# Performance work log

Hardware: AMD Instinct MI355X
Metric: run time of the kernel (lower is better)

Reference implementation:

```python
import jax, jax.numpy as jnp
import numpy as np
import math

D_MODEL = 1024
N_DEVICES = 64
HIDDEN = 128
N_HEADS = 8
B, S = 16, 1024
W_SCALE = 0.02

def setup_inputs() -> dict:
    key = jax.random.key(0)
    ks = jax.random.split(key, 24)
    f = jax.random.normal
    inp = {
        'x': f(ks[0], (B, S, D_MODEL), jnp.float32),
        # attention pooling (n_heads=8, non-causal, self-attention) weights, stored [in,out]
        'wq': f(ks[1], (D_MODEL, D_MODEL), jnp.float32) * W_SCALE,
        'bq': jnp.zeros((D_MODEL,), jnp.float32),
        'wk': f(ks[2], (D_MODEL, D_MODEL), jnp.float32) * W_SCALE,
        'bk': jnp.zeros((D_MODEL,), jnp.float32),
        'wv': f(ks[3], (D_MODEL, D_MODEL), jnp.float32) * W_SCALE,
        'bv': jnp.zeros((D_MODEL,), jnp.float32),
        'wo': f(ks[4], (D_MODEL, D_MODEL), jnp.float32) * W_SCALE,
        'bo': jnp.zeros((D_MODEL,), jnp.float32),
        # device embedding table
        'emb': f(ks[5], (N_DEVICES, D_MODEL), jnp.float32),
        # routing gate: Linear(2d,d) -> Tanh -> Linear(d,N) -> Softmax
        'rg_w1': f(ks[6], (2 * D_MODEL, D_MODEL), jnp.float32) * W_SCALE,
        'rg_b1': jnp.zeros((D_MODEL,), jnp.float32),
        'rg_w2': f(ks[7], (D_MODEL, N_DEVICES), jnp.float32) * W_SCALE,
        'rg_b2': jnp.zeros((N_DEVICES,), jnp.float32),
        'reg_w1': f(ks[8], (N_DEVICES, D_MODEL, HIDDEN), jnp.float32) * W_SCALE,
        'reg_b1': jnp.zeros((N_DEVICES, HIDDEN), jnp.float32),
        'reg_w2': f(ks[9], (N_DEVICES, HIDDEN), jnp.float32) * W_SCALE,
        'reg_b2': jnp.zeros((N_DEVICES,), jnp.float32),
        # stacked per-device classification heads: Linear(d,h)->ReLU->Linear(h,1)->Sigmoid
        'cls_w1': f(ks[10], (N_DEVICES, D_MODEL, HIDDEN), jnp.float32) * W_SCALE,
        'cls_b1': jnp.zeros((N_DEVICES, HIDDEN), jnp.float32),
        'cls_w2': f(ks[11], (N_DEVICES, HIDDEN), jnp.float32) * W_SCALE,
        'cls_b2': jnp.zeros((N_DEVICES,), jnp.float32),
    }
    return inp


def _forward(x, wq, bq, wk, bk, wv, bv, wo, bo, emb,
             rg_w1, rg_b1, rg_w2, rg_b2,
             reg_w1, reg_b1, reg_w2, reg_b2,
             cls_w1, cls_b1, cls_w2, cls_b2):
    b, s, d = x.shape
    dk = d // N_HEADS
    scale = 1.0 / math.sqrt(dk)

    def split_heads(t):  # [b,s,d] -> [b,h,s,dk]
        return t.reshape(b, s, N_HEADS, dk).transpose(0, 2, 1, 3)

    Q = split_heads(x @ wq + bq)
    K = split_heads(x @ wk + bk)
    V = split_heads(x @ wv + bv)
    scores = jnp.einsum('bhqd,bhkd->bhqk', Q, K) * scale
    attn = jax.nn.softmax(scores, axis=-1)  # non-causal, no mask, eval (no dropout)
    ctx = jnp.einsum('bhqk,bhkd->bhqd', attn, V)
    ctx = ctx.transpose(0, 2, 1, 3).reshape(b, s, d)
    pooled = ctx @ wo + bo                       # [b,s,d]
    g = pooled.mean(axis=1)                      # [b,d] global_repr

    g_exp = jnp.broadcast_to(g[:, None, :], (b, N_DEVICES, d))
    de_exp = jnp.broadcast_to(emb[None, :, :], (b, N_DEVICES, d))

    # routing gate
    ri = jnp.concatenate([g_exp, de_exp], axis=-1)        # [b,N,2d]
    h = jnp.tanh(ri @ rg_w1 + rg_b1)                      # [b,N,d]
    rw = jax.nn.softmax(h @ rg_w2 + rg_b2, axis=-1)       # [b,N,N]
    device_repr = jnp.einsum('bnm,md->bnd', rw, emb)      # bmm with expanded embeds
    combined = g_exp + device_repr                        # [b,N,d]

    hr = jax.nn.relu(jnp.einsum('bnd,ndh->bnh', combined, reg_w1) + reg_b1)
    reg = jax.nn.softplus(jnp.einsum('bnh,nh->bn', hr, reg_w2) + reg_b2)

    # per-device classification heads (stacked)
    hc = jax.nn.relu(jnp.einsum('bnd,ndh->bnh', combined, cls_w1) + cls_b1)
    cls = jax.nn.sigmoid(jnp.einsum('bnh,nh->bn', hc, cls_w2) + cls_b2)
    return reg, cls


def reference(x, wq, bq, wk, bk, wv, bv, wo, bo, emb,
              rg_w1, rg_b1, rg_w2, rg_b2,
              reg_w1, reg_b1, reg_w2, reg_b2,
              cls_w1, cls_b1, cls_w2, cls_b2):
    return _forward(x, wq, bq, wk, bk, wv, bv, wo, bo, emb,
                    rg_w1, rg_b1, rg_w2, rg_b2,
                    reg_w1, reg_b1, reg_w2, reg_b2,
                    cls_w1, cls_b1, cls_w2, cls_b2)
```

## Files before the change

### kernel.cpp

```cpp
#include <hip/hip_runtime.h>

typedef unsigned short ushort_t;
typedef __attribute__((ext_vector_type(8))) short short8;
typedef __attribute__((ext_vector_type(4))) float floatx4;

__device__ __forceinline__ ushort_t f2bf(float f) {
    unsigned u = __float_as_uint(f);
    return (ushort_t)((u + 0x7fffu + ((u >> 16) & 1u)) >> 16);
}
__device__ __forceinline__ void gll16(const void* g, void* l) {
    __builtin_amdgcn_global_load_lds(
        (const __attribute__((address_space(1))) unsigned int*)g,
        (__attribute__((address_space(3))) unsigned int*)l, 16, 0, 0);
}
#if __has_builtin(__builtin_amdgcn_exp2f)
#define EXP2f(x) __builtin_amdgcn_exp2f(x)
#else
#define EXP2f(x) exp2f(x)
#endif

__global__ void prep_kernel(const float* __restrict__ x, ushort_t* __restrict__ xb) {
    size_t i = ((size_t)blockIdx.x * 256 + threadIdx.x) * 8;
    float4 v0 = *(const float4*)(x + i);
    float4 v1 = *(const float4*)(x + i + 4);
    uint4 o;
    o.x = (unsigned)f2bf(v0.x) | ((unsigned)f2bf(v0.y) << 16);
    o.y = (unsigned)f2bf(v0.z) | ((unsigned)f2bf(v0.w) << 16);
    o.z = (unsigned)f2bf(v1.x) | ((unsigned)f2bf(v1.y) << 16);
    o.w = (unsigned)f2bf(v1.z) | ((unsigned)f2bf(v1.w) << 16);
    *(uint4*)(xb + i) = o;
}

__global__ __launch_bounds__(256) void transpose_kernel(
    const float* __restrict__ wq, const float* __restrict__ wk,
    ushort_t* __restrict__ wqT, ushort_t* __restrict__ wkT)
{
    const float* src = blockIdx.z ? wk : wq;
    ushort_t* dst = blockIdx.z ? wkT : wqT;
    const int k0 = blockIdx.x * 64, n0 = blockIdx.y * 64;
    __shared__ float t[64][65];
    const int tid = threadIdx.x;
    const int rr = tid >> 4, cc = (tid & 15) * 4;
#pragma unroll
    for (int p = 0; p < 4; ++p) {
        float4 v = *(const float4*)(src + (size_t)(k0 + p * 16 + rr) * 1024 + n0 + cc);
        t[p * 16 + rr][cc + 0] = v.x;
        t[p * 16 + rr][cc + 1] = v.y;
        t[p * 16 + rr][cc + 2] = v.z;
        t[p * 16 + rr][cc + 3] = v.w;
    }
    __syncthreads();
#pragma unroll
    for (int p = 0; p < 4; ++p) {
        int nl = p * 16 + rr;
        uint2 o;
        o.x = (unsigned)f2bf(t[cc + 0][nl]) | ((unsigned)f2bf(t[cc + 1][nl]) << 16);
        o.y = (unsigned)f2bf(t[cc + 2][nl]) | ((unsigned)f2bf(t[cc + 3][nl]) << 16);
        *(uint2*)(dst + (size_t)(n0 + nl) * 1024 + k0 + cc) = o;
    }
}

__global__ __launch_bounds__(256) void gemm_qk_kernel(
    const ushort_t* __restrict__ xb, const ushort_t* __restrict__ wqT, const ushort_t* __restrict__ wkT,
    const float* __restrict__ bq, const float* __restrict__ bk,
    ushort_t* __restrict__ Qb, ushort_t* __restrict__ Kb)
{
    const int bm = blockIdx.x;
    const int bn = blockIdx.y;
    const int mat = blockIdx.z;
    const ushort_t* W = mat ? wkT : wqT;
    const float* bias = mat ? bk : bq;
    ushort_t* Out = mat ? Kb : Qb;
    const float postscale = mat ? 1.0f : 0.12751744900508692f;

    __shared__ ushort_t a_lds[2][128 * 32];
    __shared__ ushort_t b_lds[2][128 * 32];

    const int tid = threadIdx.x;
    const int lane = tid & 63;
    const int wave = tid >> 6;
    const int wr = wave >> 1, wc = wave & 1;
    const int l16 = lane & 15, quad = lane >> 4;
    const int qs = quad ^ ((l16 >> 1) & 3);

    floatx4 acc[4][4];
    const floatx4 zero4 = {0.f, 0.f, 0.f, 0.f};
#pragma unroll
    for (int i = 0; i < 4; ++i)
#pragma unroll
        for (int j = 0; j < 4; ++j) acc[i][j] = zero4;

    const int srow = wave * 32 + (lane >> 2);
    const int skof = ((lane & 3) ^ ((lane >> 3) & 3)) * 8;
    const ushort_t* gA = xb + (size_t)(bm * 128 + srow) * 1024 + skof;
    const ushort_t* gB = W + (size_t)(bn * 128 + srow) * 1024 + skof;

    auto issue = [&](int buf, int k0) {
        ushort_t* lA = &a_lds[buf][wave * 1024];
        ushort_t* lB = &b_lds[buf][wave * 1024];
        gll16(gA + k0, lA);
        gll16(gA + k0 + 16 * 1024, lA + 512);
        gll16(gB + k0, lB);
        gll16(gB + k0 + 16 * 1024, lB + 512);
    };

    auto compute = [&](int buf) {
        const ushort_t* la = a_lds[buf];
        const ushort_t* lb = b_lds[buf];
        short8 afr[4], bfr[4];
#pragma unroll
        for (int mi = 0; mi < 4; ++mi)
            afr[mi] = *(const short8*)&la[(wr * 64 + mi * 16 + l16) * 32 + qs * 8];
#pragma unroll
        for (int ni = 0; ni < 4; ++ni)
            bfr[ni] = *(const short8*)&lb[(wc * 64 + ni * 16 + l16) * 32 + qs * 8];
#pragma unroll
        for (int mi = 0; mi < 4; ++mi)
#pragma unroll
            for (int ni = 0; ni < 4; ++ni)
                acc[mi][ni] = __builtin_amdgcn_mfma_f32_16x16x32_bf16(afr[mi], bfr[ni], acc[mi][ni], 0, 0, 0);
    };

    issue(0, 0);
#pragma unroll 4
    for (int kt = 0; kt < 31; ++kt) {
        __syncthreads();
        issue((kt + 1) & 1, (kt + 1) * 32);
        compute(kt & 1);
    }
    __syncthreads();
    compute(1);

    const int bq_ = bm >> 3;
    const int sb = (bm & 7) * 128 + wr * 64 + quad * 4;
    const int dc = wc * 64 + l16;
    float bp[4];
#pragma unroll
    for (int ni = 0; ni < 4; ++ni) bp[ni] = bias[bn * 128 + dc + ni * 16] * postscale;
    ushort_t* ob = Out + ((size_t)(bq_ * 8 + bn) * 1024 + sb) * 128 + dc;
#pragma unroll
    for (int mi = 0; mi < 4; ++mi)
#pragma unroll
        for (int ni = 0; ni < 4; ++ni) {
            ushort_t* p = ob + mi * 2048 + ni * 16;
#pragma unroll
            for (int r = 0; r < 4; ++r)
                p[r * 128] = f2bf(fmaf(acc[mi][ni][r], postscale, bp[ni]));
        }
}

__global__ __launch_bounds__(256, 4) void attn_mfma_kernel(
    const ushort_t* __restrict__ Qb,
    const ushort_t* __restrict__ Kb,
    float* __restrict__ wout)
{
    const int bh = blockIdx.x;
    const int qt = blockIdx.y;
    __shared__ ushort_t ks[2][64 * 128];

    const int tid = threadIdx.x;
    const int wave = tid >> 6, lane = tid & 63;
    const int l16 = lane & 15, quad = lane >> 4;

    const ushort_t* Ksrc = Kb + (size_t)bh * 1024 * 128;

    int srcoff[4];
#pragma unroll
    for (int c = 0; c < 4; ++c) {
        int r = wave * 16 + c * 4 + (lane >> 4);
        int g = (lane & 15) ^ (r & 15);
        srcoff[c] = r * 128 + g * 8;
    }

    auto issue = [&](int buf, int kt) {
        const ushort_t* src = Ksrc + (size_t)kt * 8192;
#pragma unroll
        for (int c = 0; c < 4; ++c)
            gll16(src + srcoff[c], &ks[buf][(wave * 4 + c) * 512]);
    };

    short8 aq[2][4];
    {
        const ushort_t* qsrc = Qb + ((size_t)bh * 1024 + qt * 128 + wave * 32) * 128;
#pragma unroll
        for (int mi = 0; mi < 2; ++mi)
#pragma unroll
            for (int ksp = 0; ksp < 4; ++ksp)
                aq[mi][ksp] = *(const short8*)(qsrc + (size_t)(mi * 16 + l16) * 128 + ksp * 32 + quad * 8);
    }

    const floatx4 zero4 = {0.f, 0.f, 0.f, 0.f};
    float lsum[2][4];
#pragma unroll
    for (int mi = 0; mi < 2; ++mi)
#pragma unroll
        for (int r = 0; r < 4; ++r) lsum[mi][r] = 0.f;

    issue(0, 0);

    for (int kt = 0; kt < 16; ++kt) {
        __syncthreads();
        if (kt < 15) issue((kt + 1) & 1, kt + 1);
        const ushort_t* kbuf = ks[kt & 1];
        floatx4 acc[2][4];
#pragma unroll
        for (int mi = 0; mi < 2; ++mi)
#pragma unroll
            for (int ni = 0; ni < 4; ++ni) acc[mi][ni] = zero4;
#pragma unroll
        for (int ksp = 0; ksp < 4; ++ksp) {
            short8 bk[4];
#pragma unroll
            for (int ni = 0; ni < 4; ++ni) {
                int n = ni * 16 + l16;
                int gs = (ksp * 4 + quad) ^ (n & 15);
                bk[ni] = *(const short8*)&kbuf[n * 128 + gs * 8];
            }
#pragma unroll
            for (int mi = 0; mi < 2; ++mi)
#pragma unroll
                for (int ni = 0; ni < 4; ++ni)
                    acc[mi][ni] = __builtin_amdgcn_mfma_f32_16x16x32_bf16(aq[mi][ksp], bk[ni], acc[mi][ni], 0, 0, 0);
        }
#pragma unroll
        for (int mi = 0; mi < 2; ++mi)
#pragma unroll
            for (int r = 0; r < 4; ++r) {
                float s = 0.f;
#pragma unroll
                for (int ni = 0; ni < 4; ++ni) s += EXP2f(acc[mi][ni][r]);
                lsum[mi][r] += s;
            }
    }

    issue(0, 0);

    float invl[2][4];
#pragma unroll
    for (int mi = 0; mi < 2; ++mi)
#pragma unroll
        for (int r = 0; r < 4; ++r) {
            float s = lsum[mi][r];
#pragma unroll
            for (int off = 1; off < 16; off <<= 1) s += __shfl_xor(s, off, 16);
            invl[mi][r] = 1.f / s;
        }

    for (int kt = 0; kt < 16; ++kt) {
        __syncthreads();
        if (kt < 15) issue((kt + 1) & 1, kt + 1);
        const ushort_t* kbuf = ks[kt & 1];
        floatx4 acc[2][4];
#pragma unroll
        for (int mi = 0; mi < 2; ++mi)
#pragma unroll
            for (int ni = 0; ni < 4; ++ni) acc[mi][ni] = zero4;
#pragma unroll
        for (int ksp = 0; ksp < 4; ++ksp) {
            short8 bk[4];
#pragma unroll
            for (int ni = 0; ni < 4; ++ni) {
                int n = ni * 16 + l16;
                int gs = (ksp * 4 + quad) ^ (n & 15);
                bk[ni] = *(const short8*)&kbuf[n * 128 + gs * 8];
            }
#pragma unroll
            for (int mi = 0; mi < 2; ++mi)
#pragma unroll
                for (int ni = 0; ni < 4; ++ni)
                    acc[mi][ni] = __builtin_amdgcn_mfma_f32_16x16x32_bf16(aq[mi][ksp], bk[ni], acc[mi][ni], 0, 0, 0);
        }
#pragma unroll
        for (int ni = 0; ni < 4; ++ni) {
            float s = 0.f;
#pragma unroll
            for (int mi = 0; mi < 2; ++mi)
#pragma unroll
                for (int r = 0; r < 4; ++r)
                    s += EXP2f(acc[mi][ni][r]) * invl[mi][r];
            s += __shfl_xor(s, 16, 64);
            s += __shfl_xor(s, 32, 64);
            if (quad == 0) atomicAdd(&wout[bh * 1024 + kt * 64 + ni * 16 + l16], s);
        }
    }
}

__global__ __launch_bounds__(256) void u_kernel(const ushort_t* __restrict__ xb,
                                                const float* __restrict__ w,
                                                float* __restrict__ u)
{
    const int b = blockIdx.x, kc = blockIdx.y;
    const int c4 = threadIdx.x;
    const ushort_t* Xp = xb + ((size_t)(b * 1024 + kc * 64)) * 1024 + c4 * 4;
    float4 acc[8];
#pragma unroll
    for (int h = 0; h < 8; ++h) acc[h] = make_float4(0.f, 0.f, 0.f, 0.f);
    const float* wb = w + b * 8 * 1024 + kc * 64;
    for (int k = 0; k < 64; ++k) {
        uint2 uv = *(const uint2*)(Xp + (size_t)k * 1024);
        float x0 = __uint_as_float(uv.x << 16);
        float x1 = __uint_as_float(uv.x & 0xffff0000u);
        float x2 = __uint_as_float(uv.y << 16);
        float x3 = __uint_as_float(uv.y & 0xffff0000u);
#pragma unroll
        for (int h = 0; h < 8; ++h) {
            float ww = wb[h * 1024 + k];
            acc[h].x = fmaf(ww, x0, acc[h].x);
            acc[h].y = fmaf(ww, x1, acc[h].y);
            acc[h].z = fmaf(ww, x2, acc[h].z);
            acc[h].w = fmaf(ww, x3, acc[h].w);
        }
    }
#pragma unroll
    for (int h = 0; h < 8; ++h) {
        float* dst = u + ((size_t)(b * 8 + h)) * 1024 + c4 * 4;
        atomicAdd(dst + 0, acc[h].x);
        atomicAdd(dst + 1, acc[h].y);
        atomicAdd(dst + 2, acc[h].z);
        atomicAdd(dst + 3, acc[h].w);
    }
}

__global__ __launch_bounds__(256) void sgemm_kernel(
    const float* __restrict__ A, int lda, long sAz,
    const float* __restrict__ Bm, int ldb, long sBz,
    const float* __restrict__ bias, long sBiasz,
    float* __restrict__ C, int ldc, long sCz,
    int M, int N, int K, float alpha, int nks)
{
    const int z = blockIdx.z;
    const int ks = blockIdx.x % nks;
    const int mt = blockIdx.x / nks;
    const int Kc = K / nks;
    A += (size_t)z * sAz;
    Bm += (size_t)z * sBz;
    C += (size_t)z * sCz;
    const float* bptr = bias ? bias + (size_t)z * sBiasz : nullptr;
    __shared__ float As[64 * 36];
    __shared__ float Bs[32 * 68];
    const int tid = threadIdx.x;
    const int row0 = mt * 64, col0 = blockIdx.y * 64;
    const int ty = tid >> 4, tx = tid & 15;
    float acc[4][4] = {};
    const int aflat = tid * 8;
    const int ar = aflat >> 5, ac = aflat & 31;
    const int br = aflat >> 6, bc = aflat & 63;
    for (int k0 = ks * Kc; k0 < (ks + 1) * Kc; k0 += 32) {
        __syncthreads();
        float4 va0 = make_float4(0.f, 0.f, 0.f, 0.f), va1 = va0;
        if (row0 + ar < M) {
            const float* src = A + (size_t)(row0 + ar) * lda + k0 + ac;
            va0 = *(const float4*)src;
            va1 = *(const float4*)(src + 4);
        }
        *(float4*)&As[ar * 36 + ac] = va0;
        *(float4*)&As[ar * 36 + ac + 4] = va1;
        {
            const float* srcb = Bm + (size_t)(k0 + br) * ldb + col0 + bc;
            *(float4*)&Bs[br * 68 + bc] = *(const float4*)srcb;
            *(float4*)&Bs[br * 68 + bc + 4] = *(const float4*)(srcb + 4);
        }
        __syncthreads();
#pragma unroll
        for (int kk = 0; kk < 32; ++kk) {
            float a0 = As[(ty * 4 + 0) * 36 + kk];
            float a1 = As[(ty * 4 + 1) * 36 + kk];
            float a2 = As[(ty * 4 + 2) * 36 + kk];
            float a3 = As[(ty * 4 + 3) * 36 + kk];
            float b0 = Bs[kk * 68 + tx * 4 + 0];
            float b1 = Bs[kk * 68 + tx * 4 + 1];
            float b2 = Bs[kk * 68 + tx * 4 + 2];
            float b3 = Bs[kk * 68 + tx * 4 + 3];
            acc[0][0] = fmaf(a0, b0, acc[0][0]); acc[0][1] = fmaf(a0, b1, acc[0][1]);
            acc[0][2] = fmaf(a0, b2, acc[0][2]); acc[0][3] = fmaf(a0, b3, acc[0][3]);
            acc[1][0] = fmaf(a1, b0, acc[1][0]); acc[1][1] = fmaf(a1, b1, acc[1][1]);
            acc[1][2] = fmaf(a1, b2, acc[1][2]); acc[1][3] = fmaf(a1, b3, acc[1][3]);
            acc[2][0] = fmaf(a2, b0, acc[2][0]); acc[2][1] = fmaf(a2, b1, acc[2][1]);
            acc[2][2] = fmaf(a2, b2, acc[2][2]); acc[2][3] = fmaf(a2, b3, acc[2][3]);
            acc[3][0] = fmaf(a3, b0, acc[3][0]); acc[3][1] = fmaf(a3, b1, acc[3][1]);
            acc[3][2] = fmaf(a3, b2, acc[3][2]); acc[3][3] = fmaf(a3, b3, acc[3][3]);
        }
    }
#pragma unroll
    for (int i = 0; i < 4; ++i) {
        int r = row0 + ty * 4 + i;
        if (r >= M) continue;
#pragma unroll
        for (int j = 0; j < 4; ++j) {
            int c = col0 + tx * 4 + j;
            float v = alpha * acc[i][j] + ((bptr && ks == 0) ? bptr[c] : 0.f);
            if (nks > 1) atomicAdd(&C[(size_t)r * ldc + c], v);
            else C[(size_t)r * ldc + c] = v;
        }
    }
}

__global__ __launch_bounds__(256) void gate_kernel(
    const float* __restrict__ Ge, const float* __restrict__ Ee, const float* __restrict__ rg_b1,
    const float* __restrict__ rg_w2, const float* __restrict__ rg_b2,
    const float* __restrict__ emb, float* __restrict__ DR)
{
    const int row = blockIdx.x;
    const int b = row >> 6, n = row & 63;
    __shared__ float h[1024];
    __shared__ float red[256];
    __shared__ float rw[64];
    const int tid = threadIdx.x;
    for (int c = tid; c < 1024; c += 256)
        h[c] = tanhf(Ge[b * 1024 + c] + Ee[n * 1024 + c] + rg_b1[c]);
    __syncthreads();
    const int j = tid & 63, ch = tid >> 6;
    float part = 0.f;
    const float* w2p = rg_w2 + (size_t)(ch * 256) * 64 + j;
    for (int c = 0; c < 256; ++c)
        part = fmaf(h[ch * 256 + c], w2p[c * 64], part);
    red[tid] = part;
    __syncthreads();
    if (tid < 64) {
        float lg = red[tid] + red[tid + 64] + red[tid + 128] + red[tid + 192] + rg_b2[j];
        float m = lg;
#pragma unroll
        for (int off = 1; off < 64; off <<= 1) m = fmaxf(m, __shfl_xor(m, off, 64));
        float e = __expf(lg - m);
        float s = e;
#pragma unroll
        for (int off = 1; off < 64; off <<= 1) s += __shfl_xor(s, off, 64);
        rw[tid] = e / s;
    }
    __syncthreads();
    float4 acc = make_float4(0.f, 0.f, 0.f, 0.f);
    const float4* E4 = (const float4*)emb;
    for (int nn = 0; nn < 64; ++nn) {
        float wv = rw[nn];
        float4 ev = E4[nn * 256 + tid];
        acc.x = fmaf(wv, ev.x, acc.x);
        acc.y = fmaf(wv, ev.y, acc.y);
        acc.z = fmaf(wv, ev.z, acc.z);
        acc.w = fmaf(wv, ev.w, acc.w);
    }
    *(float4*)&DR[(size_t)row * 1024 + tid * 4] = acc;
}

__global__ __launch_bounds__(256) void heads_p1_kernel(
    const float* __restrict__ g, const float* __restrict__ DR,
    const float* __restrict__ rw1, const float* __restrict__ cw1,
    float* __restrict__ hpart)
{
    const int n = blockIdx.x, task = blockIdx.y, ksl = blockIdx.z;
    __shared__ float combs[16 * 128];
    const int tid = threadIdx.x;
    for (int i = tid; i < 2048; i += 256) {
        int b = i >> 7, c = i & 127;
        int gc = ksl * 128 + c;
        combs[i] = g[b * 1024 + gc] + DR[((size_t)(b * 64 + n)) * 1024 + gc];
    }
    __syncthreads();
    const int j = tid & 127, sub = tid >> 7;
    const float* W1 = (task ? cw1 : rw1) + (size_t)n * 131072 + (size_t)ksl * 128 * 128;
    float a[8] = {};
    for (int c4 = 0; c4 < 32; ++c4) {
        const float w0 = W1[(c4 * 4 + 0) * 128 + j];
        const float w1 = W1[(c4 * 4 + 1) * 128 + j];
        const float w2 = W1[(c4 * 4 + 2) * 128 + j];
        const float w3 = W1[(c4 * 4 + 3) * 128 + j];
#pragma unroll
        for (int bb = 0; bb < 8; ++bb) {
            float4 cv = *(const float4*)&combs[(sub * 8 + bb) * 128 + c4 * 4];
            a[bb] = fmaf(cv.x, w0, a[bb]);
            a[bb] = fmaf(cv.y, w1, a[bb]);
            a[bb] = fmaf(cv.z, w2, a[bb]);
            a[bb] = fmaf(cv.w, w3, a[bb]);
        }
    }
    float* dst = hpart + (((size_t)(ksl * 2 + task) * 64 + n) * 16 + sub * 8) * 128 + j;
#pragma unroll
    for (int bb = 0; bb < 8; ++bb) dst[bb * 128] = a[bb];
}

__global__ __launch_bounds__(256) void heads_p2_kernel(
    const float* __restrict__ hpart,
    const float* __restrict__ rb1, const float* __restrict__ rw2, const float* __restrict__ rb2,
    const float* __restrict__ cb1, const float* __restrict__ cw2, const float* __restrict__ cb2,
    float* __restrict__ out)
{
    const int n = blockIdx.x, task = blockIdx.y;
    const int tid = threadIdx.x;
    const int b = tid >> 4, jg = tid & 15;
    const float* b1 = (task ? cb1 : rb1) + n * 128 + jg * 8;
    const float* W2 = (task ? cw2 : rw2) + n * 128 + jg * 8;
    float s = 0.f;
#pragma unroll
    for (int k = 0; k < 8; ++k) {
        float h = b1[k];
#pragma unroll
        for (int ksl = 0; ksl < 8; ++ksl)
            h += hpart[(((size_t)(ksl * 2 + task) * 64 + n) * 16 + b) * 128 + jg * 8 + k];
        s = fmaf(fmaxf(h, 0.f), W2[k], s);
    }
#pragma unroll
    for (int off = 1; off < 16; off <<= 1) s += __shfl_xor(s, off, 16);
    if (jg == 0) {
        s += (task ? cb2 : rb2)[n];
        float r = task ? (1.f / (1.f + __expf(-s)))
                       : (fmaxf(s, 0.f) + log1pf(__expf(-fabsf(s))));
        out[task * 1024 + b * 64 + n] = r;
    }
}

extern "C" void kernel_launch(void* const* d_in, const int* in_sizes, int n_in,
                              void* d_out, int out_size, void* d_ws, size_t ws_size,
                              hipStream_t stream)
{
    const float* x      = (const float*)d_in[0];
    const float* wq     = (const float*)d_in[1];
    const float* bq     = (const float*)d_in[2];
    const float* wk     = (const float*)d_in[3];
    const float* bk     = (const float*)d_in[4];
    const float* wv     = (const float*)d_in[5];
    const float* bv     = (const float*)d_in[6];
    const float* wo     = (const float*)d_in[7];
    const float* bo     = (const float*)d_in[8];
    const float* emb    = (const float*)d_in[9];
    const float* rg_w1  = (const float*)d_in[10];
    const float* rg_b1  = (const float*)d_in[11];
    const float* rg_w2  = (const float*)d_in[12];
    const float* rg_b2  = (const float*)d_in[13];
    const float* reg_w1 = (const float*)d_in[14];
    const float* reg_b1 = (const float*)d_in[15];
    const float* reg_w2 = (const float*)d_in[16];
    const float* reg_b2 = (const float*)d_in[17];
    const float* cls_w1 = (const float*)d_in[18];
    const float* cls_b1 = (const float*)d_in[19];
    const float* cls_w2 = (const float*)d_in[20];
    const float* cls_b2 = (const float*)d_in[21];

    char* ws = (char*)d_ws;
    size_t off = 0;
    auto alloc = [&](size_t bytes) { size_t cur = off; off += (bytes + 255) & ~(size_t)255; return cur; };

    ushort_t* xb  = (ushort_t*)(ws + alloc((size_t)16777216 * 2));
    ushort_t* wqT = (ushort_t*)(ws + alloc((size_t)1048576 * 2));
    ushort_t* wkT = (ushort_t*)(ws + alloc((size_t)1048576 * 2));
    ushort_t* Qb  = (ushort_t*)(ws + alloc((size_t)16777216 * 2));
    ushort_t* Kb  = (ushort_t*)(ws + alloc((size_t)16777216 * 2));
    size_t zero_beg = off;
    float* wcol = (float*)(ws + alloc((size_t)131072 * 4));
    float* u    = (float*)(ws + alloc((size_t)131072 * 4));
    float* cm   = (float*)(ws + alloc((size_t)16384 * 4));
    float* gbuf = (float*)(ws + alloc((size_t)16384 * 4));
    float* Ge   = (float*)(ws + alloc((size_t)16384 * 4));
    float* Ee   = (float*)(ws + alloc((size_t)65536 * 4));
    size_t zero_end = off;
    float* DR    = (float*)(ws + alloc((size_t)1048576 * 4));
    float* hpart = (float*)(ws + alloc((size_t)2097152 * 4));

    hipMemsetAsync(ws + zero_beg, 0, zero_end - zero_beg, stream);

    prep_kernel<<<8192, 256, 0, stream>>>(x, xb);
    transpose_kernel<<<dim3(16, 16, 2), 256, 0, stream>>>(wq, wk, wqT, wkT);
    gemm_qk_kernel<<<dim3(128, 8, 2), 256, 0, stream>>>(xb, wqT, wkT, bq, bk, Qb, Kb);
    attn_mfma_kernel<<<dim3(128, 8), 256, 0, stream>>>(Qb, Kb, wcol);
    u_kernel<<<dim3(16, 16), 256, 0, stream>>>(xb, wcol, u);
    sgemm_kernel<<<dim3(4, 2, 8), 256, 0, stream>>>(u, 8192, 1024, wv, 1024, 128, bv, 128,
                                                    cm, 1024, 128, 16, 128, 1024, 1.f / 1024.f, 4);
    sgemm_kernel<<<dim3(8, 16, 1), 256, 0, stream>>>(cm, 1024, 0, wo, 1024, 0, bo, 0,
                                                     gbuf, 1024, 0, 16, 1024, 1024, 1.f, 8);
    sgemm_kernel<<<dim3(8, 16, 1), 256, 0, stream>>>(gbuf, 1024, 0, rg_w1, 1024, 0, nullptr, 0,
                                                     Ge, 1024, 0, 16, 1024, 1024, 1.f, 8);
    sgemm_kernel<<<dim3(8, 16, 1), 256, 0, stream>>>(emb, 1024, 0, rg_w1 + (size_t)1048576, 1024, 0, nullptr, 0,
                                                     Ee, 1024, 0, 64, 1024, 1024, 1.f, 8);
    gate_kernel<<<1024, 256, 0, stream>>>(Ge, Ee, rg_b1, rg_w2, rg_b2, emb, DR);
    heads_p1_kernel<<<dim3(64, 2, 8), 256, 0, stream>>>(gbuf, DR, reg_w1, cls_w1, hpart);
    heads_p2_kernel<<<dim3(64, 2), 256, 0, stream>>>(hpart, reg_b1, reg_w2, reg_b2,
                                                     cls_b1, cls_w2, cls_b2, (float*)d_out);
    (void)in_sizes; (void)n_in; (void)out_size; (void)ws_size;
}
```

Baseline: 524.9 us.

## Fuse prep/transpose launches, share X tile across Q/K GEMM, widen attention blocks

Merges the x bf16 conversion and the weight transposes into one launch. Rewrites the Q/K projection GEMM as 512-thread blocks that load the x tile once and compute both Q and K, which halves A-tile traffic. Doubles the attention block size to 8 waves covering 256 query rows, so each staged K tile is shared by more queries. Also merges the two routing-gate sgemm launches into one kernel. The cost is higher LDS and register pressure per block and fewer, larger blocks. The attention kernel body beyond the load indexing is not visible, so its consistency with the new 256-row tile cannot be fully checked.

```diff
diff --git a/kernel.cpp b/kernel.cpp
--- a/kernel.cpp
+++ b/kernel.cpp
@@ -19,27 +19,31 @@
 #define EXP2f(x) exp2f(x)
 #endif
 
-__global__ void prep_kernel(const float* __restrict__ x, ushort_t* __restrict__ xb) {
-    size_t i = ((size_t)blockIdx.x * 256 + threadIdx.x) * 8;
-    float4 v0 = *(const float4*)(x + i);
-    float4 v1 = *(const float4*)(x + i + 4);
-    uint4 o;
-    o.x = (unsigned)f2bf(v0.x) | ((unsigned)f2bf(v0.y) << 16);
-    o.y = (unsigned)f2bf(v0.z) | ((unsigned)f2bf(v0.w) << 16);
-    o.z = (unsigned)f2bf(v1.x) | ((unsigned)f2bf(v1.y) << 16);
-    o.w = (unsigned)f2bf(v1.z) | ((unsigned)f2bf(v1.w) << 16);
-    *(uint4*)(xb + i) = o;
-}
-
-__global__ __launch_bounds__(256) void transpose_kernel(
+__global__ __launch_bounds__(256) void prep_tr_kernel(
+    const float* __restrict__ x, ushort_t* __restrict__ xb,
     const float* __restrict__ wq, const float* __restrict__ wk,
     ushort_t* __restrict__ wqT, ushort_t* __restrict__ wkT)
 {
-    const float* src = blockIdx.z ? wk : wq;
-    ushort_t* dst = blockIdx.z ? wkT : wqT;
-    const int k0 = blockIdx.x * 64, n0 = blockIdx.y * 64;
     __shared__ float t[64][65];
-    const int tid = threadIdx.x;
+    const int bid = blockIdx.x;
+    const int tid = threadIdx.x;
+    if (bid < 8192) {
+        size_t i = ((size_t)bid * 256 + tid) * 8;
+        float4 v0 = *(const float4*)(x + i);
+        float4 v1 = *(const float4*)(x + i + 4);
+        uint4 o;
+        o.x = (unsigned)f2bf(v0.x) | ((unsigned)f2bf(v0.y) << 16);
+        o.y = (unsigned)f2bf(v0.z) | ((unsigned)f2bf(v0.w) << 16);
+        o.z = (unsigned)f2bf(v1.x) | ((unsigned)f2bf(v1.y) << 16);
+        o.w = (unsigned)f2bf(v1.z) | ((unsigned)f2bf(v1.w) << 16);
+        *(uint4*)(xb + i) = o;
+        return;
+    }
+    const int b2 = bid - 8192;
+    const int bx = b2 & 15, by = (b2 >> 4) & 15, bz = b2 >> 8;
+    const float* src = bz ? wk : wq;
+    ushort_t* dst = bz ? wkT : wqT;
+    const int k0 = bx * 64, n0 = by * 64;
     const int rr = tid >> 4, cc = (tid & 15) * 4;
 #pragma unroll
     for (int p = 0; p < 4; ++p) {
@@ -60,26 +64,23 @@
     }
 }
 
-__global__ __launch_bounds__(256) void gemm_qk_kernel(
+__global__ __launch_bounds__(512, 4) void gemm_qk_kernel(
     const ushort_t* __restrict__ xb, const ushort_t* __restrict__ wqT, const ushort_t* __restrict__ wkT,
     const float* __restrict__ bq, const float* __restrict__ bk,
     ushort_t* __restrict__ Qb, ushort_t* __restrict__ Kb)
 {
     const int bm = blockIdx.x;
     const int bn = blockIdx.y;
-    const int mat = blockIdx.z;
-    const ushort_t* W = mat ? wkT : wqT;
-    const float* bias = mat ? bk : bq;
-    ushort_t* Out = mat ? Kb : Qb;
-    const float postscale = mat ? 1.0f : 0.12751744900508692f;
 
     __shared__ ushort_t a_lds[2][128 * 32];
-    __shared__ ushort_t b_lds[2][128 * 32];
+    __shared__ ushort_t q_lds[2][128 * 32];
+    __shared__ ushort_t k_lds[2][128 * 32];
 
     const int tid = threadIdx.x;
     const int lane = tid & 63;
     const int wave = tid >> 6;
-    const int wr = wave >> 1, wc = wave & 1;
+    const int wmat = wave >> 2;
+    const int wr = (wave >> 1) & 1, wc = wave & 1;
     const int l16 = lane & 15, quad = lane >> 4;
     const int qs = quad ^ ((l16 >> 1) & 3);
 
@@ -90,23 +91,24 @@
 #pragma unroll
         for (int j = 0; j < 4; ++j) acc[i][j] = zero4;
 
-    const int srow = wave * 32 + (lane >> 2);
-    const int skof = ((lane & 3) ^ ((lane >> 3) & 3)) * 8;
+    const int srow = tid >> 2;
+    const int skof = ((tid & 3) ^ ((tid >> 3) & 3)) * 8;
     const ushort_t* gA = xb + (size_t)(bm * 128 + srow) * 1024 + skof;
-    const ushort_t* gB = W + (size_t)(bn * 128 + srow) * 1024 + skof;
+    const ushort_t* gQ = wqT + (size_t)(bn * 128 + srow) * 1024 + skof;
+    const ushort_t* gK = wkT + (size_t)(bn * 128 + srow) * 1024 + skof;
 
     auto issue = [&](int buf, int k0) {
-        ushort_t* lA = &a_lds[buf][wave * 1024];
-        ushort_t* lB = &b_lds[buf][wave * 1024];
-        gll16(gA + k0, lA);
-        gll16(gA + k0 + 16 * 1024, lA + 512);
-        gll16(gB + k0, lB);
-        gll16(gB + k0 + 16 * 1024, lB + 512);
+        gll16(gA + k0, &a_lds[buf][wave * 512]);
+        gll16(gQ + k0, &q_lds[buf][wave * 512]);
+        gll16(gK + k0, &k_lds[buf][wave * 512]);
     };
+
+    const ushort_t* lbase = wmat ? k_lds[0] : q_lds[0];
+    const int lstride = wmat ? (int)(k_lds[1] - k_lds[0]) : (int)(q_lds[1] - q_lds[0]);
 
     auto compute = [&](int buf) {
         const ushort_t* la = a_lds[buf];
-        const ushort_t* lb = b_lds[buf];
+        const ushort_t* lb = lbase + buf * lstride;
         short8 afr[4], bfr[4];
 #pragma unroll
         for (int mi = 0; mi < 4; ++mi)
@@ -131,6 +133,10 @@
     __syncthreads();
     compute(1);
 
+    ushort_t* Out = wmat ? Kb : Qb;
+    const float* bias = wmat ? bk : bq;
+    const float postscale = wmat ? 1.0f : 0.12751744900508692f;
+
     const int bq_ = bm >> 3;
     const int sb = (bm & 7) * 128 + wr * 64 + quad * 4;
     const int dc = wc * 64 + l16;
@@ -149,7 +155,7 @@
         }
 }
 
-__global__ __launch_bounds__(256, 4) void attn_mfma_kernel(
+__global__ __launch_bounds__(512, 4) void attn_mfma_kernel(
     const ushort_t* __restrict__ Qb,
     const ushort_t* __restrict__ Kb,
     float* __restrict__ wout)
@@ -164,24 +170,24 @@
 
     const ushort_t* Ksrc = Kb + (size_t)bh * 1024 * 128;
 
-    int srcoff[4];
-#pragma unroll
-    for (int c = 0; c < 4; ++c) {
-        int r = wave * 16 + c * 4 + (lane >> 4);
-        int g = (lane & 15) ^ (r & 15);
+    int srcoff[2];
+#pragma unroll
+    for (int c = 0; c < 2; ++c) {
+        int r = c * 32 + (tid >> 4);
+        int g = (tid & 15) ^ (r & 15);
         srcoff[c] = r * 128 + g * 8;
     }
 
     auto issue = [&](int buf, int kt) {
         const ushort_t* src = Ksrc + (size_t)kt * 8192;
 #pragma unroll
-        for (int c = 0; c < 4; ++c)
-            gll16(src + srcoff[c], &ks[buf][(wave * 4 + c) * 512]);
+        for (int c = 0; c < 2; ++c)
+            gll16(src + srcoff[c], &ks[buf][c * 4096 + wave * 512]);
     };
 
     short8 aq[2][4];
     {
-        const ushort_t* qsrc = Qb + ((size_t)bh * 1024 + qt * 128 + wave * 32) * 128;
+        const ushort_t* qsrc = Qb + ((size_t)bh * 1024 + qt * 256 + wave * 32) * 128;
 #pragma unroll
         for (int mi = 0; mi < 2; ++mi)
 #pragma unroll
@@ -391,6 +397,74 @@
             float v = alpha * acc[i][j] + ((bptr && ks == 0) ? bptr[c] : 0.f);
             if (nks > 1) atomicAdd(&C[(size_t)r * ldc + c], v);
             else C[(size_t)r * ldc + c] = v;
+        }
+    }
+}
+
+__global__ __launch_bounds__(256) void sgemm_ge_ee_kernel(
+    const float* __restrict__ gbuf, const float* __restrict__ emb,
+    const float* __restrict__ rg_w1, float* __restrict__ Ge, float* __restrict__ Ee)
+{
+    const int z = blockIdx.z;
+    const float* A = z ? emb : gbuf;
+    const float* Bm = rg_w1 + (size_t)z * 1048576;
+    float* C = z ? Ee : Ge;
+    const int M = z ? 64 : 16;
+    const int nks = 8, Kc = 128;
+    const int ks = blockIdx.x % nks;
+    __shared__ float As[64 * 36];
+    __shared__ float Bs[32 * 68];
+    const int tid = threadIdx.x;
+    const int col0 = blockIdx.y * 64;
+    const int ty = tid >> 4, tx = tid & 15;
+    float acc[4][4] = {};
+    const int aflat = tid * 8;
+    const int ar = aflat >> 5, ac = aflat & 31;
+    const int br = aflat >> 6, bc = aflat & 63;
+    for (int k0 = ks * Kc; k0 < (ks + 1) * Kc; k0 += 32) {
+        __syncthreads();
+        float4 va0 = make_float4(0.f, 0.f, 0.f, 0.f), va1 = va0;
+        if (ar < M) {
+            const float* src = A + (size_t)ar * 1024 + k0 + ac;
+            va0 = *(const float4*)src;
+            va1 = *(const float4*)(src + 4);
+        }
+        *(float4*)&As[ar * 36 + ac] = va0;
+        *(float4*)&As[ar * 36 + ac + 4] = va1;
+        {
+            const float* srcb = Bm + (size_t)(k0 + br) * 1024 + col0 + bc;
+            *(float4*)&Bs[br * 68 + bc] = *(const float4*)srcb;
+            *(float4*)&Bs[br * 68 + bc + 4] = *(const float4*)(srcb + 4);
+        }
+        __syncthreads();
+#pragma unroll
+        for (int kk = 0; kk < 32; ++kk) {
+            float a0 = As[(ty * 4 + 0) * 36 + kk];
+            float a1 = As[(ty * 4 + 1) * 36 + kk];
+            float a2 = As[(ty * 4 + 2) * 36 + kk];
+            float a3 = As[(ty * 4 + 3) * 36 + kk];
+            float b0 = Bs[kk * 68 + tx * 4 + 0];
+            float b1 = Bs[kk * 68 + tx * 4 + 1];
+            float b2 = Bs[kk * 68 + tx * 4 + 2];
+            float b3 = Bs[kk * 68 + tx * 4 + 3];
+            acc[0][0] = fmaf(a0, b0, acc[0][0]); acc[0][1] = fmaf(a0, b1, acc[0][1]);
+            acc[0][2] = fmaf(a0, b2, acc[0][2]); acc[0][3] = fmaf(a0, b3, acc[0][3]);
+            acc[1][0] = fmaf(a1, b0, acc[1][0]); acc[1][1] = fmaf(a1, b1, acc[1][1]);
+            acc[1][2] = fmaf(a1, b2, acc[1][2]); acc[1][3] = fmaf(a1, b3, acc[1][3]);
+            acc[2][0] = fmaf(a2, b0, acc[2][0]); acc[2][1] = fmaf(a2, b1, acc[2][1]);
+            acc[2][2] = fmaf(a2, b2, acc[2][2]); acc[2][3] = fmaf(a2, b3, acc[2][3]);
+            acc[3][0] = fmaf(a3, b0, acc[3][0]); acc[3][1] = fmaf(a3, b1, acc[3][1]);
+            acc[3][2] = fmaf(a3, b2, acc[3][2]); acc[3][3] = fmaf(a3, b3, acc[3][3]);
+        }
+    }
+#pragma unroll
+    for (int i = 0; i < 4; ++i) {
+        int r = ty * 4 + i;
+        if (r >= M) continue;
+#pragma unroll
+        for (int j = 0; j < 4; ++j) {
+            int c = col0 + tx * 4 + j;
+            atomicAdd(&C[(size_t)r * 1024 + c], acc[i][j]);
         }
     }
 }
@@ -556,19 +630,15 @@
 
     hipMemsetAsync(ws + zero_beg, 0, zero_end - zero_beg, stream);
 
-    prep_kernel<<<8192, 256, 0, stream>>>(x, xb);
-    transpose_kernel<<<dim3(16, 16, 2), 256, 0, stream>>>(wq, wk, wqT, wkT);
-    gemm_qk_kernel<<<dim3(128, 8, 2), 256, 0, stream>>>(xb, wqT, wkT, bq, bk, Qb, Kb);
-    attn_mfma_kernel<<<dim3(128, 8), 256, 0, stream>>>(Qb, Kb, wcol);
+    prep_tr_kernel<<<8704, 256, 0, stream>>>(x, xb, wq, wk, wqT, wkT);
+    gemm_qk_kernel<<<dim3(128, 8), 512, 0, stream>>>(xb, wqT, wkT, bq, bk, Qb, Kb);
+    attn_mfma_kernel<<<dim3(128, 4), 512, 0, stream>>>(Qb, Kb, wcol);
     u_kernel<<<dim3(16, 16), 256, 0, stream>>>(xb, wcol, u);
     sgemm_kernel<<<dim3(4, 2, 8), 256, 0, stream>>>(u, 8192, 1024, wv, 1024, 128, bv, 128,
                                                     cm, 1024, 128, 16, 128, 1024, 1.f / 1024.f, 4);
     sgemm_kernel<<<dim3(8, 16, 1), 256, 0, stream>>>(cm, 1024, 0, wo, 1024, 0, bo, 0,
                                                      gbuf, 1024, 0, 16, 1024, 1024, 1.f, 8);
-    sgemm_kernel<<<dim3(8, 16, 1), 256, 0, stream>>>(gbuf, 1024, 0, rg_w1, 1024, 0, nullptr, 0,
-                                                     Ge, 1024, 0, 16, 1024, 1024, 1.f, 8);
-    sgemm_kernel<<<dim3(8, 16, 1), 256, 0, stream>>>(emb, 1024, 0, rg_w1 + (size_t)1048576, 1024, 0, nullptr, 0,
-                                                     Ee, 1024, 0, 64, 1024, 1024, 1.f, 8);
+    sgemm_ge_ee_kernel<<<dim3(8, 16, 2), 256, 0, stream>>>(gbuf, emb, rg_w1, Ge, Ee);
     gate_kernel<<<1024, 256, 0, stream>>>(Ge, Ee, rg_b1, rg_w2, rg_b2, emb, DR);
     heads_p1_kernel<<<dim3(64, 2, 8), 256, 0, stream>>>(gbuf, DR, reg_w1, cls_w1, hpart);
     heads_p2_kernel<<<dim3(64, 2), 256, 0, stream>>>(hpart, reg_b1, reg_w2, reg_b2,
```

New measurement: 487.0 us. 7.2% less time.
